# Optimization experiments

Hardware: AMD Instinct MI355X
Metric: run time of the kernel (lower is better)

Reference implementation:

```python
import jax, jax.numpy as jnp
import numpy as np

N_LAYERS = 2  # BasicEntanglerLayers depth of the qlayer surrogate
N_WIRES = 4
CNOT_RING = [(0, 1), (1, 2), (2, 3), (3, 0)]


def _ry(state, q, theta):
    # state: (N, 2, 2, 2, 2) real statevector; RY is a real 2x2 rotation.
    N = state.shape[0]
    theta = jnp.broadcast_to(jnp.asarray(theta, state.dtype), (N,)).reshape(N, 1, 1, 1)
    c, s = jnp.cos(theta * 0.5), jnp.sin(theta * 0.5)
    s0 = jax.lax.index_in_dim(state, 0, q + 1, keepdims=False)  # (N,2,2,2)
    s1 = jax.lax.index_in_dim(state, 1, q + 1, keepdims=False)
    return jnp.stack([c * s0 - s * s1, s * s0 + c * s1], axis=q + 1)


def _cnot(state, c, t):
    # flip target axis on the control=1 slab
    s0 = jax.lax.index_in_dim(state, 0, c + 1, keepdims=True)
    s1 = jax.lax.index_in_dim(state, 1, c + 1, keepdims=True)
    return jnp.concatenate([s0, jnp.flip(s1, axis=t + 1)], axis=c + 1)


def _qcircuit(xblk, qweights):
    # xblk: (N, 4) embedding angles; qweights: (L, 4). Returns expval Z0, shape (N,).
    N = xblk.shape[0]
    state = jnp.zeros((N, 2, 2, 2, 2), xblk.dtype).at[:, 0, 0, 0, 0].set(1.0)
    for i in range(N_WIRES):                      # AngleEmbedding (RY)
        state = _ry(state, i, xblk[:, i])
    for l in range(N_LAYERS):                     # BasicEntanglerLayers
        for i in range(N_WIRES):
            state = _ry(state, i, qweights[l, i])
        for c, t in CNOT_RING:
            state = _cnot(state, c, t)
    p = state * state
    return p[:, 0].sum(axis=(1, 2, 3)) - p[:, 1].sum(axis=(1, 2, 3))


def _filtering(x):
    # (B, 784) -> (B*14*14, 4): 2x2 blocks of the 28x28 image
    B = x.shape[0]
    return x.reshape(B, 14, 2, 14, 2).transpose(0, 1, 3, 2, 4).reshape(B * 196, 4)


def setup_inputs() -> dict:
    key = jax.random.key(0)
    ks = jax.random.split(key, 6)
    B = 4096
    return {
        "x": jax.random.uniform(ks[0], (B, 784), jnp.float32),
        "qweights": jax.random.normal(ks[1], (N_LAYERS, N_WIRES), jnp.float32),
        "W1": jax.random.normal(ks[2], (196, 30), jnp.float32) * (1.0 / np.sqrt(196)),
        "b1": jax.random.normal(ks[3], (30,), jnp.float32) * 0.01,
        "W2": jax.random.normal(ks[4], (30, 2), jnp.float32) * (1.0 / np.sqrt(30)),
        "b2": jax.random.normal(ks[5], (2,), jnp.float32) * 0.01,
    }


def reference(x, qweights, W1, b1, W2, b2):
    B = x.shape[0]
    blocks = _filtering(x)                 # (B*196, 4)
    z = _qcircuit(blocks, qweights)        # (B*196,) — batched over all blocks
    h = z.reshape(B, 196)
    h = jnp.maximum(h @ W1 + b1, 0.0)      # Linear(196,30) + ReLU
    return h @ W2 + b2                     # Linear(30,2)
```

## Files before the change

### kernel.cpp

```cpp
#include <hip/hip_runtime.h>


__global__ __launch_bounds__(256) void hybrid_qnn_kernel(
    const float* __restrict__ x,
    const float* __restrict__ qw,
    const float* __restrict__ W1,
    const float* __restrict__ b1,
    const float* __restrict__ W2,
    const float* __restrict__ b2,
    float* __restrict__ out)
{
    __shared__ float lx[784];
    __shared__ float lz[196];
    __shared__ float lh[32];
    __shared__ float cw[8];
    __shared__ float sw[8];

    const int img = blockIdx.x;
    const int t   = threadIdx.x;

    const float* xi = x + (size_t)img * 784;
    #pragma unroll
    for (int k = 0; k < 4; ++k) {
        int idx = t + k * 256;
        if (idx < 784) lx[idx] = xi[idx];
    }
    if (t < 8) {
        float c, s;
        sincosf(0.5f * qw[t], &s, &c);
        cw[t] = c; sw[t] = s;
    }
    __syncthreads();

    if (t < 196) {
        const int i = t / 14;
        const int j = t - 14 * i;
        const int base = i * 56 + j * 2;
        float c0,s0,c1,s1,c2,s2,c3,s3;
        sincosf(0.5f * lx[base],      &s0, &c0);
        sincosf(0.5f * lx[base + 1],  &s1, &c1);
        sincosf(0.5f * lx[base + 28], &s2, &c2);
        sincosf(0.5f * lx[base + 29], &s3, &c3);

        float st[16];
        {
            float f01[4] = {c0*c1, c0*s1, s0*c1, s0*s1};
            float f23[4] = {c2*c3, c2*s3, s2*c3, s2*s3};
            #pragma unroll
            for (int a = 0; a < 4; ++a)
                #pragma unroll
                for (int b = 0; b < 4; ++b)
                    st[a*4+b] = f01[a] * f23[b];
        }

#define RY_GATE(MASK, C, S) { \
        _Pragma("unroll") \
        for (int idx = 0; idx < 16; ++idx) { \
            if (!(idx & (MASK))) { \
                float u0 = st[idx], u1 = st[idx | (MASK)]; \
                st[idx]          = (C)*u0 - (S)*u1; \
                st[idx | (MASK)] = (S)*u0 + (C)*u1; \
            } \
        } }

#define CNOT_GATE(CM, TM) { \
        _Pragma("unroll") \
        for (int idx = 0; idx < 16; ++idx) { \
            if ((idx & (CM)) && !(idx & (TM))) { \
                float tmp = st[idx]; st[idx] = st[idx | (TM)]; st[idx | (TM)] = tmp; \
            } \
        } }

        #pragma unroll
        for (int l = 0; l < 2; ++l) {
            RY_GATE(8, cw[l*4+0], sw[l*4+0]);
            RY_GATE(4, cw[l*4+1], sw[l*4+1]);
            RY_GATE(2, cw[l*4+2], sw[l*4+2]);
            RY_GATE(1, cw[l*4+3], sw[l*4+3]);
            CNOT_GATE(8, 4);
            CNOT_GATE(4, 2);
            CNOT_GATE(2, 1);
            CNOT_GATE(1, 8);
        }

        float zp = 0.f, zn = 0.f;
        #pragma unroll
        for (int idx = 0; idx < 8; ++idx)  zp = fmaf(st[idx], st[idx], zp);
        #pragma unroll
        for (int idx = 8; idx < 16; ++idx) zn = fmaf(st[idx], st[idx], zn);
        lz[t] = zp - zn;
#undef RY_GATE
#undef CNOT_GATE
    }
    __syncthreads();

    if (t < 30) {
        float acc = b1[t];
        #pragma unroll 4
        for (int j = 0; j < 196; ++j)
            acc = fmaf(lz[j], W1[j * 30 + t], acc);
        lh[t] = fmaxf(acc, 0.f);
    }
    __syncthreads();

    if (t < 2) {
        float acc = b2[t];
        #pragma unroll
        for (int k = 0; k < 30; ++k)
            acc = fmaf(lh[k], W2[k * 2 + t], acc);
        out[img * 2 + t] = acc;
    }
}

extern "C" void kernel_launch(void* const* d_in, const int* in_sizes, int n_in,
                              void* d_out, int out_size, void* d_ws, size_t ws_size,
                              hipStream_t stream) {
    const float* x  = (const float*)d_in[0];
    const float* qw = (const float*)d_in[1];
    const float* W1 = (const float*)d_in[2];
    const float* b1 = (const float*)d_in[3];
    const float* W2 = (const float*)d_in[4];
    const float* b2 = (const float*)d_in[5];
    float* out = (float*)d_out;

    const int B = in_sizes[0] / 784;
    hipLaunchKernelGGL(hybrid_qnn_kernel, dim3(B), dim3(256), 0, stream,
                       x, qw, W1, b1, W2, b2, out);
}
```

Measured before the change: 94.89 us.

## Load pixels directly, use fast sincos, and split the W1 dot product across threads

Each thread now reads its 2x2 pixel block straight from global memory with float2 loads instead of staging the whole image in shared memory. Every thread computes the weight sincos itself, which removes one barrier. Fast __sincosf intrinsics replace the precise sincosf. The 196x30 hidden layer is spread over 240 threads (8 segments per output) with shuffle reductions, where before only 30 threads each ran a serial 196-step loop. The cost is reduced trig accuracy and redundant weight trig per thread.

Result: faster. 85.71 us (-9.7%).

```diff
diff --git a/kernel.cpp b/kernel.cpp
--- a/kernel.cpp
+++ b/kernel.cpp
@@ -10,37 +10,29 @@
     const float* __restrict__ b2,
     float* __restrict__ out)
 {
-    __shared__ float lx[784];
     __shared__ float lz[196];
-    __shared__ float lh[32];
-    __shared__ float cw[8];
-    __shared__ float sw[8];
+    __shared__ float lh[30];
 
     const int img = blockIdx.x;
     const int t   = threadIdx.x;
 
-    const float* xi = x + (size_t)img * 784;
-    #pragma unroll
-    for (int k = 0; k < 4; ++k) {
-        int idx = t + k * 256;
-        if (idx < 784) lx[idx] = xi[idx];
-    }
-    if (t < 8) {
-        float c, s;
-        sincosf(0.5f * qw[t], &s, &c);
-        cw[t] = c; sw[t] = s;
-    }
-    __syncthreads();
-
     if (t < 196) {
         const int i = t / 14;
         const int j = t - 14 * i;
-        const int base = i * 56 + j * 2;
+        const float* xp = x + (size_t)img * 784 + i * 56 + j * 2;
+        const float2 r0 = *(const float2*)xp;
+        const float2 r1 = *(const float2*)(xp + 28);
+
         float c0,s0,c1,s1,c2,s2,c3,s3;
-        sincosf(0.5f * lx[base],      &s0, &c0);
-        sincosf(0.5f * lx[base + 1],  &s1, &c1);
-        sincosf(0.5f * lx[base + 28], &s2, &c2);
-        sincosf(0.5f * lx[base + 29], &s3, &c3);
+        __sincosf(0.5f * r0.x, &s0, &c0);
+        __sincosf(0.5f * r0.y, &s1, &c1);
+        __sincosf(0.5f * r1.x, &s2, &c2);
+        __sincosf(0.5f * r1.y, &s3, &c3);
+
+        float cw[8], sw[8];
+        #pragma unroll
+        for (int k = 0; k < 8; ++k)
+            __sincosf(0.5f * qw[k], &sw[k], &cw[k]);
 
         float st[16];
         {
@@ -82,6 +74,8 @@
             CNOT_GATE(2, 1);
             CNOT_GATE(1, 8);
         }
+#undef RY_GATE
+#undef CNOT_GATE
 
         float zp = 0.f, zn = 0.f;
         #pragma unroll
@@ -89,17 +83,22 @@
         #pragma unroll
         for (int idx = 8; idx < 16; ++idx) zn = fmaf(st[idx], st[idx], zn);
         lz[t] = zp - zn;
-#undef RY_GATE
-#undef CNOT_GATE
     }
     __syncthreads();
 
-    if (t < 30) {
-        float acc = b1[t];
-        #pragma unroll 4
-        for (int j = 0; j < 196; ++j)
-            acc = fmaf(lz[j], W1[j * 30 + t], acc);
-        lh[t] = fmaxf(acc, 0.f);
+    if (t < 240) {
+        const int o   = t >> 3;
+        const int seg = t & 7;
+        float acc = 0.f;
+        #pragma unroll
+        for (int i = 0; i < 25; ++i) {
+            const int j = seg * 25 + i;
+            if (j < 196) acc = fmaf(lz[j], W1[j * 30 + o], acc);
+        }
+        acc += __shfl_down(acc, 4, 8);
+        acc += __shfl_down(acc, 2, 8);
+        acc += __shfl_down(acc, 1, 8);
+        if (seg == 0) lh[o] = fmaxf(acc + b1[o], 0.f);
     }
     __syncthreads();
 
```
